# Performance work log

Hardware: AMD Instinct MI355X
Metric: run time of the kernel (lower is better)

## Reference

```python
import jax, jax.numpy as jnp
import numpy as np

L, H, D, E, V, MAXS = 12, 12, 64, 768, 50257, 1024

def _ln(x, g, b, eps=1e-5):
    m = jnp.mean(x, axis=-1, keepdims=True)
    v = jnp.mean(jnp.square(x - m), axis=-1, keepdims=True)
    return (x - m) * jax.lax.rsqrt(v + eps) * g + b

def setup_inputs() -> dict:
    key = jax.random.key(0)
    ks = jax.random.split(key, 16)
    s = 0.02
    inp = {
        "input_ids": jax.random.randint(ks[0], (1, 1), 0, V),
        "past_key": jax.random.normal(ks[1], (L, 1, H, MAXS, D), jnp.float32),
        "past_value": jax.random.normal(ks[2], (L, 1, H, MAXS, D), jnp.float32),
        "past_seq_len": 1023,
        "attention_mask": jnp.ones((1, MAXS), jnp.float32),
        "wte": jax.random.normal(ks[3], (V, E), jnp.float32) * s,
        "wpe": jax.random.normal(ks[4], (MAXS, E), jnp.float32) * s,
        "ln1_g": jnp.ones((L, E), jnp.float32),
        "ln1_b": jnp.zeros((L, E), jnp.float32),
        "attn_w": jax.random.normal(ks[5], (L, E, 3 * E), jnp.float32) * s,
        "attn_b": jnp.zeros((L, 3 * E), jnp.float32),
        "proj_w": jax.random.normal(ks[6], (L, E, E), jnp.float32) * s,
        "proj_b": jnp.zeros((L, E), jnp.float32),
        "ln2_g": jnp.ones((L, E), jnp.float32),
        "ln2_b": jnp.zeros((L, E), jnp.float32),
        "fc_w": jax.random.normal(ks[7], (L, E, 4 * E), jnp.float32) * s,
        "fc_b": jnp.zeros((L, 4 * E), jnp.float32),
        "mlp_w": jax.random.normal(ks[8], (L, 4 * E, E), jnp.float32) * s,
        "mlp_b": jnp.zeros((L, E), jnp.float32),
        "lnf_g": jnp.ones((E,), jnp.float32),
        "lnf_b": jnp.zeros((E,), jnp.float32),
    }
    return inp

def reference(input_ids, past_key, past_value, past_seq_len, attention_mask,
              wte, wpe, ln1_g, ln1_b, attn_w, attn_b, proj_w, proj_b,
              ln2_g, ln2_b, fc_w, fc_b, mlp_w, mlp_b, lnf_g, lnf_b):
    S = int(past_seq_len)  # static cache length
    h = wte[input_ids] + wpe[S]                      # [1,1,E]
    bias = (1.0 - attention_mask[:, :S + 1]) * -1e9  # [1,S+1]
    scale = 1.0 / jnp.sqrt(jnp.float32(D))
    pk, pv = past_key, past_value
    for l in range(L):
        x = _ln(h, ln1_g[l], ln1_b[l])
        qkv = x @ attn_w[l] + attn_b[l]              # [1,1,3E]
        q, k, v = jnp.split(qkv, 3, axis=-1)
        q = q.reshape(1, 1, H, D).transpose(0, 2, 1, 3)  # [1,H,1,D]
        k = k.reshape(1, 1, H, D).transpose(0, 2, 1, 3)
        v = v.reshape(1, 1, H, D).transpose(0, 2, 1, 3)
        k_full = jnp.concatenate([pk[l, :, :, :S, :], k], axis=2)  # [1,H,S+1,D]
        v_full = jnp.concatenate([pv[l, :, :, :S, :], v], axis=2)
        scores = jnp.einsum('bhqd,bhkd->bhqk', q, k_full) * scale
        scores = scores + bias[:, None, None, :]
        attn = jax.nn.softmax(scores, axis=-1)
        o = jnp.einsum('bhqk,bhkd->bhqd', attn, v_full)
        o = o.transpose(0, 2, 1, 3).reshape(1, 1, H * D)
        h = h + o @ proj_w[l] + proj_b[l]
        x2 = _ln(h, ln2_g[l], ln2_b[l])
        h = h + jax.nn.gelu(x2 @ fc_w[l] + fc_b[l], approximate=True) @ mlp_w[l] + mlp_b[l]
        pk = pk.at[l, :, :, S, :].set(k[:, :, 0, :])
        pv = pv.at[l, :, :, S, :].set(v[:, :, 0, :])
    h = _ln(h, lnf_g, lnf_b)
    logits = h @ wte.T                               # [1,1,V] (tied lm_head)
    return (logits, pk, pv)
```

## Files before the change

### kernel.cpp

```cpp
#include <hip/hip_runtime.h>
#include <math.h>

#define EMB 768
#define NH 12
#define HD 64
#define NL 12
#define NV 50257
#define MAXS 1024
#define S_PAST 1023
#define E3 2304
#define E4 3072

#define WS_HA   0
#define WS_HB   768
#define WS_QKV  1536
#define WS_FC   3840
#define WS_Y    6912
#define WS_T    16128

__device__ __forceinline__ void f4add(float4& a, const float4& b) {
  a.x += b.x; a.y += b.y; a.z += b.z; a.w += b.w;
}
__device__ __forceinline__ void f4fma(float4& a, float x, const float4& w) {
  a.x += x * w.x; a.y += x * w.y; a.z += x * w.z; a.w += x * w.w;
}

__device__ __forceinline__ void blockReduce2(float& a, float& b, volatile float* ra, volatile float* rb) {
  int lane = threadIdx.x & 63, wid = threadIdx.x >> 6;
#pragma unroll
  for (int o = 32; o > 0; o >>= 1) { a += __shfl_down(a, o); b += __shfl_down(b, o); }
  if (lane == 0) { ra[wid] = a; rb[wid] = b; }
  __syncthreads();
  if (threadIdx.x == 0) {
    ra[0] = ra[0] + ra[1] + ra[2] + ra[3];
    rb[0] = rb[0] + rb[1] + rb[2] + rb[3];
  }
  __syncthreads();
  a = ra[0]; b = rb[0];
}

__device__ __forceinline__ float gelu(float x) {
  return 0.5f * x * (1.f + tanhf(0.7978845608028654f * (x + 0.044715f * x * x * x)));
}

__global__ void init_kernel(const int* __restrict__ ids, const float* __restrict__ wte,
                            const float* __restrict__ wpe, const float* __restrict__ attn_b,
                            float* __restrict__ wsf) {
  int tid = threadIdx.x, bi = blockIdx.x;
  if (bi < 9) {
    wsf[WS_QKV + bi * 256 + tid] = attn_b[bi * 256 + tid];
  } else {
    int e = (bi - 9) * 256 + tid;
    int id = ids[0];
    wsf[WS_HA + e] = wte[(size_t)id * EMB + e] + wpe[(size_t)S_PAST * EMB + e];
  }
}

__global__ void ln_gemv4(const float* __restrict__ hvec, const float* __restrict__ g,
                         const float* __restrict__ bb, const float* __restrict__ W,
                         float* __restrict__ out, const float* __restrict__ fc_b,
                         float* __restrict__ wsf, int l) {
  __shared__ float lh[EMB];
  __shared__ float xs[32];
  __shared__ float ra[4], rb[4];
  __shared__ float4 red[4][64];
  int tid = threadIdx.x, lane = tid & 63, wid = tid >> 6;
  int e0 = blockIdx.y * 32;
  float hv0 = hvec[tid], hv1 = hvec[tid + 256], hv2 = hvec[tid + 512];
  int j4 = blockIdx.x * 64 + lane;
  const int N4 = E3 >> 2;
  const float4* p = (const float4*)(W + (size_t)l * EMB * E3) + (size_t)(e0 + wid) * N4 + j4;
  float4 w[8];
#pragma unroll
  for (int i = 0; i < 8; i++) w[i] = p[(size_t)(i * 4) * N4];
  if (blockIdx.y == 1) {
    int t0 = blockIdx.x * 256 + tid;
    for (int i = t0; i < 9228; i += 2304) wsf[WS_Y + i] = 0.f;
  } else if (blockIdx.y == 2) {
    int t0 = blockIdx.x * 256 + tid;
    for (int i = t0; i < E4; i += 2304) wsf[WS_FC + i] = fc_b[l * E4 + i];
  }
  float gv = 0.f, bv = 0.f;
  if (tid < 32) { gv = g[l * EMB + e0 + tid]; bv = bb[l * EMB + e0 + tid]; }
  lh[tid] = hv0; lh[tid + 256] = hv1; lh[tid + 512] = hv2;
  float s1 = hv0 + hv1 + hv2;
  float s2 = hv0 * hv0 + hv1 * hv1 + hv2 * hv2;
  blockReduce2(s1, s2, ra, rb);
  float mean = s1 * (1.f / EMB);
  float var = s2 * (1.f / EMB) - mean * mean;
  float rstd = rsqrtf(var + 1e-5f);
  if (tid < 32) xs[tid] = (lh[e0 + tid] - mean) * rstd * gv + bv;
  __syncthreads();
  float4 acc = {0.f, 0.f, 0.f, 0.f};
#pragma unroll
  for (int i = 0; i < 8; i++) f4fma(acc, xs[wid + i * 4], w[i]);
  red[wid][lane] = acc;
  __syncthreads();
  if (wid == 0) {
    float4 a0 = red[0][lane], a1 = red[1][lane], a2 = red[2][lane], a3 = red[3][lane];
    float rx = a0.x + a1.x + a2.x + a3.x;
    float ry = a0.y + a1.y + a2.y + a3.y;
    float rz = a0.z + a1.z + a2.z + a3.z;
    float rw = a0.w + a1.w + a2.w + a3.w;
    float* op = out + (size_t)j4 * 4;
    atomicAdd(op + 0, rx); atomicAdd(op + 1, ry);
    atomicAdd(op + 2, rz); atomicAdd(op + 3, rw);
  }
}

__global__ __launch_bounds__(256) void attn_kv(
    const float* __restrict__ qkv, const float* __restrict__ pk,
    const float* __restrict__ pv, const float* __restrict__ mask,
    const float* __restrict__ proj_w, float* __restrict__ opk, float* __restrict__ opv,
    float* __restrict__ wsf, int l) {
  int g = (blockIdx.x & 7) * 24 + (blockIdx.x >> 3);
  int h = g >> 4, c = g & 15;
  int tid = threadIdx.x, lane = tid & 63, wid = tid >> 6;
  int sub = tid & 15, grp = tid >> 4;
  __shared__ float4 qs4[16];
  __shared__ float sc[64];
  __shared__ float oc[64];
  __shared__ float4 redo[4][16];
  if (tid < 16) qs4[tid] = ((const float4*)(qkv + h * 64))[tid];
  __syncthreads();
  size_t base = ((size_t)(l * NH + h) * MAXS) * HD;
  const float4* K4 = (const float4*)(pk + base);
  const float4* V4 = (const float4*)(pv + base);
  float4* oK4 = (float4*)(opk + base);
  float4* oV4 = (float4*)(opv + base);
  int t0 = c * 64;
  float4 kreg[4];
#pragma unroll
  for (int i = 0; i < 4; i++) {
    int t = t0 + grp + i * 16;
    kreg[i] = (t == S_PAST) ? ((const float4*)(qkv + EMB + h * 64))[sub] : K4[(size_t)t * 16 + sub];
  }
#pragma unroll
  for (int i = 0; i < 4; i++) {
    int t = t0 + grp + i * 16;
    oK4[(size_t)t * 16 + sub] = kreg[i];
  }
  float4 q4 = qs4[sub];
#pragma unroll
  for (int i = 0; i < 4; i++) {
    int key = grp + i * 16;
    float p = q4.x * kreg[i].x + q4.y * kreg[i].y + q4.z * kreg[i].z + q4.w * kreg[i].w;
    p += __shfl_xor(p, 1); p += __shfl_xor(p, 2);
    p += __shfl_xor(p, 4); p += __shfl_xor(p, 8);
    if (sub == 0) sc[key] = p * 0.125f + (1.f - mask[t0 + key]) * (-1e9f);
  }
  __syncthreads();
  if (wid == 0) {
    float e = expf(sc[lane]);
    sc[lane] = e;
    float s = e;
#pragma unroll
    for (int o = 32; o > 0; o >>= 1) s += __shfl_down(s, o);
    if (lane == 0) atomicAdd(wsf + WS_T + h, s);
  }
  __syncthreads();
  float4 vreg[4];
#pragma unroll
  for (int i = 0; i < 4; i++) {
    int t = t0 + grp + i * 16;
    vreg[i] = (t == S_PAST) ? ((const float4*)(qkv + 2 * EMB + h * 64))[sub] : V4[(size_t)t * 16 + sub];
  }
#pragma unroll
  for (int i = 0; i < 4; i++) {
    int t = t0 + grp + i * 16;
    oV4[(size_t)t * 16 + sub] = vreg[i];
  }
  float4 acc = {0.f, 0.f, 0.f, 0.f};
#pragma unroll
  for (int i = 0; i < 4; i++) f4fma(acc, sc[grp + i * 16], vreg[i]);
  acc.x += __shfl_xor(acc.x, 16); acc.y += __shfl_xor(acc.y, 16);
  acc.z += __shfl_xor(acc.z, 16); acc.w += __shfl_xor(acc.w, 16);
  acc.x += __shfl_xor(acc.x, 32); acc.y += __shfl_xor(acc.y, 32);
  acc.z += __shfl_xor(acc.z, 32); acc.w += __shfl_xor(acc.w, 32);
  if (lane < 16) redo[wid][lane] = acc;
  __syncthreads();
  if (tid < 16) {
    float4 a0 = redo[0][tid], a1 = redo[1][tid], a2 = redo[2][tid], a3 = redo[3][tid];
    float4 r;
    r.x = a0.x + a1.x + a2.x + a3.x;
    r.y = a0.y + a1.y + a2.y + a3.y;
    r.z = a0.z + a1.z + a2.z + a3.z;
    r.w = a0.w + a1.w + a2.w + a3.w;
    ((float4*)oc)[tid] = r;
  }
  __syncthreads();
  if (tid < 192) {
    const float4* Wp4 = (const float4*)(proj_w + (size_t)l * EMB * EMB)
                        + (size_t)h * 64 * (EMB >> 2) + tid;
    float4 pa = {0.f, 0.f, 0.f, 0.f};
#pragma unroll
    for (int b = 0; b < 4; b++) {
      float4 w[16];
#pragma unroll
      for (int i = 0; i < 16; i++) w[i] = Wp4[(size_t)(b * 16 + i) * (EMB >> 2)];
#pragma unroll
      for (int i = 0; i < 16; i++) f4fma(pa, oc[b * 16 + i], w[i]);
    }
    float* yp = wsf + WS_Y + h * EMB + tid * 4;
    atomicAdd(yp + 0, pa.x); atomicAdd(yp + 1, pa.y);
    atomicAdd(yp + 2, pa.z); atomicAdd(yp + 3, pa.w);
  }
}

__global__ void fc_gemv(const float* __restrict__ R, float* __restrict__ S,
                        const float* __restrict__ proj_b, const float* __restrict__ g2,
                        const float* __restrict__ b2, const float* __restrict__ W,
                        float* __restrict__ wsf, int l) {
  __shared__ float lh[EMB];
  __shared__ float xs[32];
  __shared__ float ra[4], rb[4];
  __shared__ float4 red[4][64];
  int tid = threadIdx.x, lane = tid & 63, wid = tid >> 6;
  int jt = blockIdx.x, et = blockIdx.y, e0 = et * 32;
  int j4 = jt * 64 + lane;
  const int N4 = E4 >> 2;
  const float4* p = (const float4*)(W + (size_t)l * EMB * E4) + (size_t)(e0 + wid) * N4 + j4;
  float4 w[8];
#pragma unroll
  for (int i = 0; i < 8; i++) w[i] = p[(size_t)(i * 4) * N4];
  float invT[NH];
#pragma unroll
  for (int hh = 0; hh < NH; hh++) invT[hh] = 1.f / wsf[WS_T + hh];
  float hn[3];
#pragma unroll
  for (int k = 0; k < 3; k++) {
    int e = tid + 256 * k;
    float v = R[e] + proj_b[l * EMB + e];
#pragma unroll
    for (int hh = 0; hh < NH; hh++) v += wsf[WS_Y + hh * EMB + e] * invT[hh];
    hn[k] = v;
    lh[e] = v;
  }
  if (jt == 0 && et == 0) {
#pragma unroll
    for (int k = 0; k < 3; k++) S[tid + 256 * k] = hn[k];
  }
  float gv = 0.f, bv = 0.f;
  if (tid < 32) { gv = g2[l * EMB + e0 + tid]; bv = b2[l * EMB + e0 + tid]; }
  float s1 = hn[0] + hn[1] + hn[2];
  float s2 = hn[0] * hn[0] + hn[1] * hn[1] + hn[2] * hn[2];
  blockReduce2(s1, s2, ra, rb);
  float mean = s1 * (1.f / EMB);
  float var = s2 * (1.f / EMB) - mean * mean;
  float rstd = rsqrtf(var + 1e-5f);
  if (tid < 32) xs[tid] = (lh[e0 + tid] - mean) * rstd * gv + bv;
  __syncthreads();
  float4 acc = {0.f, 0.f, 0.f, 0.f};
#pragma unroll
  for (int i = 0; i < 8; i++) f4fma(acc, xs[wid + i * 4], w[i]);
  red[wid][lane] = acc;
  __syncthreads();
  if (wid == 0) {
    float4 a0 = red[0][lane], a1 = red[1][lane], a2 = red[2][lane], a3 = red[3][lane];
    float rx = a0.x + a1.x + a2.x + a3.x;
    float ry = a0.y + a1.y + a2.y + a3.y;
    float rz = a0.z + a1.z + a2.z + a3.z;
    float rw = a0.w + a1.w + a2.w + a3.w;
    float* op = wsf + WS_FC + (size_t)j4 * 4;
    atomicAdd(op + 0, rx); atomicAdd(op + 1, ry);
    atomicAdd(op + 2, rz); atomicAdd(op + 3, rw);
  }
}

__global__ void mlp_gemv4(const float* __restrict__ fcv, const float* __restrict__ W,
                          const float* __restrict__ bias, const float* __restrict__ attn_b,
                          float* __restrict__ hout, float* __restrict__ qkv, int l) {
  __shared__ float xs[64];
  __shared__ float4 red[4][64];
  int tid = threadIdx.x, lane = tid & 63, wid = tid >> 6;
  int e0 = blockIdx.y * 64;
  int j4 = blockIdx.x * 64 + lane;
  const int N4 = EMB >> 2;
  const float4* p = (const float4*)(W + (size_t)l * E4 * EMB) + (size_t)(e0 + wid) * N4 + j4;
  float4 w[16];
#pragma unroll
  for (int i = 0; i < 16; i++) w[i] = p[(size_t)(i * 4) * N4];
  if (tid < 64) xs[tid] = gelu(fcv[e0 + tid]);
  int bid = blockIdx.y * 3 + blockIdx.x;
  if (l + 1 < NL && bid < 9) qkv[bid * 256 + tid] = attn_b[(l + 1) * E3 + bid * 256 + tid];
  __syncthreads();
  float4 acc = {0.f, 0.f, 0.f, 0.f};
#pragma unroll
  for (int i = 0; i < 16; i++) f4fma(acc, xs[wid + i * 4], w[i]);
  red[wid][lane] = acc;
  __syncthreads();
  if (wid == 0) {
    float4 a0 = red[0][lane], a1 = red[1][lane], a2 = red[2][lane], a3 = red[3][lane];
    float rx = a0.x + a1.x + a2.x + a3.x;
    float ry = a0.y + a1.y + a2.y + a3.y;
    float rz = a0.z + a1.z + a2.z + a3.z;
    float rw = a0.w + a1.w + a2.w + a3.w;
    if (blockIdx.y == 0) {
      const float* bp = bias + l * EMB + j4 * 4;
      rx += bp[0]; ry += bp[1]; rz += bp[2]; rw += bp[3];
    }
    float* op = hout + (size_t)j4 * 4;
    atomicAdd(op + 0, rx); atomicAdd(op + 1, ry);
    atomicAdd(op + 2, rz); atomicAdd(op + 3, rw);
  }
}

__global__ void logits_lnf(const float* __restrict__ hvec, const float* __restrict__ g,
                           const float* __restrict__ b, const float* __restrict__ wte,
                           float* __restrict__ out) {
  __shared__ __align__(16) float4 xs4[192];
  __shared__ float ra[4], rb[4];
  int tid = threadIdx.x, lane = tid & 63, wid = tid >> 6;
  float hv0 = hvec[tid], hv1 = hvec[tid + 256], hv2 = hvec[tid + 512];
  int v = blockIdx.x * 4 + wid;
  float4 a0 = {0,0,0,0}, a1 = {0,0,0,0}, a2 = {0,0,0,0};
  if (v < NV) {
    const float4* row = (const float4*)(wte + (size_t)v * EMB);
    a0 = row[lane]; a1 = row[lane + 64]; a2 = row[lane + 128];
  }
  float s1 = hv0 + hv1 + hv2;
  float s2 = hv0 * hv0 + hv1 * hv1 + hv2 * hv2;
  blockReduce2(s1, s2, ra, rb);
  float mean = s1 * (1.f / EMB);
  float var = s2 * (1.f / EMB) - mean * mean;
  float rstd = rsqrtf(var + 1e-5f);
  ((float*)xs4)[tid]       = (hv0 - mean) * rstd * g[tid]       + b[tid];
  ((float*)xs4)[tid + 256] = (hv1 - mean) * rstd * g[tid + 256] + b[tid + 256];
  ((float*)xs4)[tid + 512] = (hv2 - mean) * rstd * g[tid + 512] + b[tid + 512];
  __syncthreads();
  if (v >= NV) return;
  float4 x0 = xs4[lane], x1 = xs4[lane + 64], x2 = xs4[lane + 128];
  float acc = a0.x * x0.x + a0.y * x0.y + a0.z * x0.z + a0.w * x0.w
            + a1.x * x1.x + a1.y * x1.y + a1.z * x1.z + a1.w * x1.w
            + a2.x * x2.x + a2.y * x2.y + a2.z * x2.z + a2.w * x2.w;
#pragma unroll
  for (int o = 32; o > 0; o >>= 1) acc += __shfl_down(acc, o);
  if (lane == 0) out[v] = acc;
}

extern "C" void kernel_launch(void* const* d_in, const int* in_sizes, int n_in,
                              void* d_out, int out_size, void* d_ws, size_t ws_size,
                              hipStream_t stream) {
  const int* input_ids = (const int*)d_in[0];
  const float* past_key = (const float*)d_in[1];
  const float* past_value = (const float*)d_in[2];
  const float* mask = (const float*)d_in[4];
  const float* wte = (const float*)d_in[5];
  const float* wpe = (const float*)d_in[6];
  const float* ln1_g = (const float*)d_in[7];
  const float* ln1_b = (const float*)d_in[8];
  const float* attn_w = (const float*)d_in[9];
  const float* attn_b = (const float*)d_in[10];
  const float* proj_w = (const float*)d_in[11];
  const float* proj_b = (const float*)d_in[12];
  const float* ln2_g = (const float*)d_in[13];
  const float* ln2_b = (const float*)d_in[14];
  const float* fc_w = (const float*)d_in[15];
  const float* fc_b = (const float*)d_in[16];
  const float* mlp_w = (const float*)d_in[17];
  const float* mlp_b = (const float*)d_in[18];
  const float* lnf_g = (const float*)d_in[19];
  const float* lnf_b = (const float*)d_in[20];

  float* out = (float*)d_out;
  float* out_logits = out;
  float* out_pk = out + NV;
  float* out_pv = out_pk + (size_t)NL * NH * MAXS * HD;

  float* wsf = (float*)d_ws;
  float* wqkv = wsf + WS_QKV;
  float* wfc = wsf + WS_FC;

  init_kernel<<<12, 256, 0, stream>>>(input_ids, wte, wpe, attn_b, wsf);

  for (int l = 0; l < NL; l++) {
    float* R = wsf + ((l & 1) ? WS_HB : WS_HA);
    float* S = wsf + ((l & 1) ? WS_HA : WS_HB);
    ln_gemv4<<<dim3(9, 24), 256, 0, stream>>>(R, ln1_g, ln1_b, attn_w, wqkv, fc_b, wsf, l);
    attn_kv<<<192, 256, 0, stream>>>(wqkv, past_key, past_value, mask, proj_w,
                                     out_pk, out_pv, wsf, l);
    fc_gemv<<<dim3(12, 24), 256, 0, stream>>>(R, S, proj_b, ln2_g, ln2_b, fc_w, wsf, l);
    mlp_gemv4<<<dim3(3, 48), 256, 0, stream>>>(wfc, mlp_w, mlp_b, attn_b, S, wqkv, l);
  }
  logits_lnf<<<12565, 256, 0, stream>>>(wsf + WS_HA, lnf_g, lnf_b, wte, out_logits);
}
```

Baseline: 458.8 us.

## Add spare prefetch blocks that pull upcoming weights and KV cache into cache

Each kernel launch gets extra blocks that only read the weights or KV slices needed by the next stage or layer, such as proj/fc during QKV, mlp during attention, and next-layer attn_w and KV during MLP. The goal is to warm the large last-level cache so the dependent GEMV and attention kernels read from cache instead of HBM. Grids become 1D with the block index decoded by hand. The cost is extra HBM traffic and CU occupancy that competes with the real work. The gain depends on the prefetched data staying resident until it is used.

```diff
diff --git a/kernel.cpp b/kernel.cpp
--- a/kernel.cpp
+++ b/kernel.cpp
@@ -18,11 +18,26 @@
 #define WS_Y    6912
 #define WS_T    16128
 
+#define L_ATTNW (EMB * E3)
+#define L_FCW   (EMB * E4)
+#define L_KV    (NH * MAXS * HD)
+
 __device__ __forceinline__ void f4add(float4& a, const float4& b) {
   a.x += b.x; a.y += b.y; a.z += b.z; a.w += b.w;
 }
 __device__ __forceinline__ void f4fma(float4& a, float x, const float4& w) {
   a.x += x * w.x; a.y += x * w.y; a.z += x * w.z; a.w += x * w.w;
+}
+
+__device__ __forceinline__ void pf_range(const float* p, size_t nf, int pi, int nb) {
+  const float4* p4 = (const float4*)p;
+  size_t n4 = nf >> 2;
+  float acc = 0.f;
+  for (size_t i = (size_t)pi * 256 + threadIdx.x; i < n4; i += (size_t)nb * 256) {
+    float4 v = p4[i];
+    acc += v.x + v.y + v.z + v.w;
+  }
+  asm volatile("" :: "v"(acc));
 }
 
 __device__ __forceinline__ void blockReduce2(float& a, float& b, volatile float* ra, volatile float* rb) {
@@ -45,40 +60,53 @@
 
 __global__ void init_kernel(const int* __restrict__ ids, const float* __restrict__ wte,
                             const float* __restrict__ wpe, const float* __restrict__ attn_b,
-                            float* __restrict__ wsf) {
+                            const float* __restrict__ attn_w, const float* __restrict__ pk,
+                            const float* __restrict__ pv, float* __restrict__ wsf) {
   int tid = threadIdx.x, bi = blockIdx.x;
   if (bi < 9) {
     wsf[WS_QKV + bi * 256 + tid] = attn_b[bi * 256 + tid];
-  } else {
+  } else if (bi < 12) {
     int e = (bi - 9) * 256 + tid;
     int id = ids[0];
     wsf[WS_HA + e] = wte[(size_t)id * EMB + e] + wpe[(size_t)S_PAST * EMB + e];
+  } else if (bi < 76) {
+    pf_range(attn_w, L_ATTNW, bi - 12, 64);
+  } else if (bi < 124) {
+    pf_range(pk, L_KV, bi - 76, 48);
+  } else {
+    pf_range(pv, L_KV, bi - 124, 48);
   }
 }
 
 __global__ void ln_gemv4(const float* __restrict__ hvec, const float* __restrict__ g,
                          const float* __restrict__ bb, const float* __restrict__ W,
                          float* __restrict__ out, const float* __restrict__ fc_b,
+                         const float* __restrict__ proj_w, const float* __restrict__ fc_w,
                          float* __restrict__ wsf, int l) {
+  int bi = blockIdx.x;
+  if (bi >= 216) {
+    if (bi < 248) pf_range(proj_w + (size_t)l * EMB * EMB, EMB * EMB, bi - 216, 32);
+    else pf_range(fc_w + (size_t)l * L_FCW, L_FCW / 2, bi - 248, 64);
+    return;
+  }
+  int jt = bi % 9, et = bi / 9;
   __shared__ float lh[EMB];
   __shared__ float xs[32];
   __shared__ float ra[4], rb[4];
   __shared__ float4 red[4][64];
   int tid = threadIdx.x, lane = tid & 63, wid = tid >> 6;
-  int e0 = blockIdx.y * 32;
+  int e0 = et * 32;
   float hv0 = hvec[tid], hv1 = hvec[tid + 256], hv2 = hvec[tid + 512];
-  int j4 = blockIdx.x * 64 + lane;
+  int j4 = jt * 64 + lane;
   const int N4 = E3 >> 2;
   const float4* p = (const float4*)(W + (size_t)l * EMB * E3) + (size_t)(e0 + wid) * N4 + j4;
   float4 w[8];
 #pragma unroll
   for (int i = 0; i < 8; i++) w[i] = p[(size_t)(i * 4) * N4];
-  if (blockIdx.y == 1) {
-    int t0 = blockIdx.x * 256 + tid;
-    for (int i = t0; i < 9228; i += 2304) wsf[WS_Y + i] = 0.f;
-  } else if (blockIdx.y == 2) {
-    int t0 = blockIdx.x * 256 + tid;
-    for (int i = t0; i < E4; i += 2304) wsf[WS_FC + i] = fc_b[l * E4 + i];
+  if (et == 1) {
+    for (int i = jt * 256 + tid; i < 9228; i += 2304) wsf[WS_Y + i] = 0.f;
+  } else if (et == 2) {
+    for (int i = jt * 256 + tid; i < E4; i += 2304) wsf[WS_FC + i] = fc_b[l * E4 + i];
   }
   float gv = 0.f, bv = 0.f;
   if (tid < 32) { gv = g[l * EMB + e0 + tid]; bv = bb[l * EMB + e0 + tid]; }
@@ -111,9 +139,16 @@
 __global__ __launch_bounds__(256) void attn_kv(
     const float* __restrict__ qkv, const float* __restrict__ pk,
     const float* __restrict__ pv, const float* __restrict__ mask,
-    const float* __restrict__ proj_w, float* __restrict__ opk, float* __restrict__ opv,
+    const float* __restrict__ proj_w, const float* __restrict__ fc_w,
+    const float* __restrict__ mlp_w, float* __restrict__ opk, float* __restrict__ opv,
     float* __restrict__ wsf, int l) {
-  int g = (blockIdx.x & 7) * 24 + (blockIdx.x >> 3);
+  int bi = blockIdx.x;
+  if (bi >= 192) {
+    if (bi < 248) pf_range(fc_w + (size_t)l * L_FCW + L_FCW / 2, L_FCW / 2, bi - 192, 56);
+    else pf_range(mlp_w + (size_t)l * L_FCW, L_FCW / 2, bi - 248, 56);
+    return;
+  }
+  int g = (bi & 7) * 24 + (bi >> 3);
   int h = g >> 4, c = g & 15;
   int tid = threadIdx.x, lane = tid & 63, wid = tid >> 6;
   int sub = tid & 15, grp = tid >> 4;
@@ -210,13 +245,22 @@
 __global__ void fc_gemv(const float* __restrict__ R, float* __restrict__ S,
                         const float* __restrict__ proj_b, const float* __restrict__ g2,
                         const float* __restrict__ b2, const float* __restrict__ W,
-                        float* __restrict__ wsf, int l) {
+                        const float* __restrict__ mlp_w, const float* __restrict__ attn_w,
+                        const float* __restrict__ wte, float* __restrict__ wsf, int l) {
+  int bi = blockIdx.x;
+  if (bi >= 288) {
+    if (bi < 336) pf_range(mlp_w + (size_t)l * L_FCW + L_FCW / 2, L_FCW / 2, bi - 288, 48);
+    else if (l + 1 < NL) pf_range(attn_w + (size_t)(l + 1) * L_ATTNW, L_ATTNW / 2, bi - 336, 48);
+    else pf_range(wte, L_ATTNW, bi - 336, 48);
+    return;
+  }
+  int jt = bi % 12, et = bi / 12;
   __shared__ float lh[EMB];
   __shared__ float xs[32];
   __shared__ float ra[4], rb[4];
   __shared__ float4 red[4][64];
   int tid = threadIdx.x, lane = tid & 63, wid = tid >> 6;
-  int jt = blockIdx.x, et = blockIdx.y, e0 = et * 32;
+  int e0 = et * 32;
   int j4 = jt * 64 + lane;
   const int N4 = E4 >> 2;
   const float4* p = (const float4*)(W + (size_t)l * EMB * E4) + (size_t)(e0 + wid) * N4 + j4;
@@ -236,7 +280,7 @@
     hn[k] = v;
     lh[e] = v;
   }
-  if (jt == 0 && et == 0) {
+  if (bi == 0) {
 #pragma unroll
     for (int k = 0; k < 3; k++) S[tid + 256 * k] = hn[k];
   }
@@ -269,20 +313,37 @@
 
 __global__ void mlp_gemv4(const float* __restrict__ fcv, const float* __restrict__ W,
                           const float* __restrict__ bias, const float* __restrict__ attn_b,
+                          const float* __restrict__ attn_w, const float* __restrict__ pk,
+                          const float* __restrict__ pv, const float* __restrict__ wte,
                           float* __restrict__ hout, float* __restrict__ qkv, int l) {
+  int bi = blockIdx.x;
+  if (bi >= 144) {
+    if (bi < 200) {
+      if (l + 1 < NL) pf_range(attn_w + (size_t)(l + 1) * L_ATTNW + L_ATTNW / 2, L_ATTNW / 2, bi - 144, 56);
+      else pf_range(wte + L_ATTNW, L_ATTNW, bi - 144, 56);
+    } else {
+      if (l + 1 < NL) {
+        if (bi < 228) pf_range(pk + (size_t)(l + 1) * L_KV, L_KV, bi - 200, 28);
+        else pf_range(pv + (size_t)(l + 1) * L_KV, L_KV, bi - 228, 28);
+      } else {
+        pf_range(wte + 2 * L_ATTNW, 2 * L_ATTNW, bi - 200, 56);
+      }
+    }
+    return;
+  }
+  int jt3 = bi % 3, et2 = bi / 3;
   __shared__ float xs[64];
   __shared__ float4 red[4][64];
   int tid = threadIdx.x, lane = tid & 63, wid = tid >> 6;
-  int e0 = blockIdx.y * 64;
-  int j4 = blockIdx.x * 64 + lane;
+  int e0 = et2 * 64;
+  int j4 = jt3 * 64 + lane;
   const int N4 = EMB >> 2;
   const float4* p = (const float4*)(W + (size_t)l * E4 * EMB) + (size_t)(e0 + wid) * N4 + j4;
   float4 w[16];
 #pragma unroll
   for (int i = 0; i < 16; i++) w[i] = p[(size_t)(i * 4) * N4];
   if (tid < 64) xs[tid] = gelu(fcv[e0 + tid]);
-  int bid = blockIdx.y * 3 + blockIdx.x;
-  if (l + 1 < NL && bid < 9) qkv[bid * 256 + tid] = attn_b[(l + 1) * E3 + bid * 256 + tid];
+  if (l + 1 < NL && bi < 9) qkv[bi * 256 + tid] = attn_b[(l + 1) * E3 + bi * 256 + tid];
   __syncthreads();
   float4 acc = {0.f, 0.f, 0.f, 0.f};
 #pragma unroll
@@ -295,7 +356,7 @@
     float ry = a0.y + a1.y + a2.y + a3.y;
     float rz = a0.z + a1.z + a2.z + a3.z;
     float rw = a0.w + a1.w + a2.w + a3.w;
-    if (blockIdx.y == 0) {
+    if (et2 == 0) {
       const float* bp = bias + l * EMB + j4 * 4;
       rx += bp[0]; ry += bp[1]; rz += bp[2]; rw += bp[3];
     }
@@ -371,16 +432,20 @@
   float* wqkv = wsf + WS_QKV;
   float* wfc = wsf + WS_FC;
 
-  init_kernel<<<12, 256, 0, stream>>>(input_ids, wte, wpe, attn_b, wsf);
+  init_kernel<<<172, 256, 0, stream>>>(input_ids, wte, wpe, attn_b, attn_w,
+                                       past_key, past_value, wsf);
 
   for (int l = 0; l < NL; l++) {
     float* R = wsf + ((l & 1) ? WS_HB : WS_HA);
     float* S = wsf + ((l & 1) ? WS_HA : WS_HB);
-    ln_gemv4<<<dim3(9, 24), 256, 0, stream>>>(R, ln1_g, ln1_b, attn_w, wqkv, fc_b, wsf, l);
-    attn_kv<<<192, 256, 0, stream>>>(wqkv, past_key, past_value, mask, proj_w,
-                                     out_pk, out_pv, wsf, l);
-    fc_gemv<<<dim3(12, 24), 256, 0, stream>>>(R, S, proj_b, ln2_g, ln2_b, fc_w, wsf, l);
-    mlp_gemv4<<<dim3(3, 48), 256, 0, stream>>>(wfc, mlp_w, mlp_b, attn_b, S, wqkv, l);
+    ln_gemv4<<<312, 256, 0, stream>>>(R, ln1_g, ln1_b, attn_w, wqkv, fc_b,
+                                      proj_w, fc_w, wsf, l);
+    attn_kv<<<304, 256, 0, stream>>>(wqkv, past_key, past_value, mask, proj_w,
+                                     fc_w, mlp_w, out_pk, out_pv, wsf, l);
+    fc_gemv<<<384, 256, 0, stream>>>(R, S, proj_b, ln2_g, ln2_b, fc_w,
+                                     mlp_w, attn_w, wte, wsf, l);
+    mlp_gemv4<<<256, 256, 0, stream>>>(wfc, mlp_w, mlp_b, attn_b, attn_w,
+                                       past_key, past_value, wte, S, wqkv, l);
   }
   logits_lnf<<<12565, 256, 0, stream>>>(wsf + WS_HA, lnf_g, lnf_b, wte, out_logits);
 }
```

After: 760.5 us. 65.8% more time.
